# Performance work log

Hardware: AMD Instinct MI355X
Metric: run time of the kernel (lower is better)

## Reference

```python
import jax, jax.numpy as jnp
import numpy as np

B, N, C = 8, 1024, 1024
H = 16
D = C // H  # head_dim = 64
SCALE = D ** -0.5


def setup_inputs() -> dict:
    key = jax.random.key(0)
    k1, k2, k3 = jax.random.split(key, 3)
    x = jax.random.normal(k1, (B, N, C), dtype=jnp.float32)
    w_qkv = jax.random.normal(k2, (3 * C, C), dtype=jnp.float32) * (C ** -0.5)
    w_proj = jax.random.normal(k3, (C, C), dtype=jnp.float32) * (C ** -0.5)
    b_proj = jnp.zeros((C,), dtype=jnp.float32)
    return {"x": x, "w_qkv": w_qkv, "w_proj": w_proj, "b_proj": b_proj}


def reference(x, w_qkv, w_proj, b_proj):
    Bx, Nx, Cx = x.shape
    # qkv: [B,N,3C] -> [3,B,H,N,D]
    qkv = jnp.einsum('bnc,oc->bno', x, w_qkv)
    qkv = qkv.reshape(Bx, Nx, 3, H, D).transpose(2, 0, 3, 1, 4)
    q, k, v = qkv[0], qkv[1], qkv[2]
    attn = jnp.einsum('bhnd,bhmd->bhnm', q, k) * SCALE  # [B,H,N,N]
    attn = jax.nn.softmax(attn, axis=-1)
    out = jnp.einsum('bhnm,bhmd->bhnd', attn, v)  # [B,H,N,D]
    out = out.transpose(0, 2, 1, 3).reshape(Bx, Nx, Cx)
    return jnp.einsum('bnc,oc->bno', out, w_proj) + b_proj
```

## Files before the change

### kernel.cpp

```cpp
#include <hip/hip_runtime.h>

typedef _Float16 half8 __attribute__((ext_vector_type(8)));
typedef _Float16 half4v __attribute__((ext_vector_type(4)));
typedef _Float16 half2v __attribute__((ext_vector_type(2)));
typedef float floatx4 __attribute__((ext_vector_type(4)));

#define AS3 __attribute__((address_space(3)))
#define AS1 __attribute__((address_space(1)))

__global__ __launch_bounds__(256) void cvt_all(const float* __restrict__ x,
                                               const float* __restrict__ wq,
                                               const float* __restrict__ wp,
                                               _Float16* __restrict__ xh,
                                               _Float16* __restrict__ wqh,
                                               _Float16* __restrict__ wph) {
    long i = (long)blockIdx.x * 256 + threadIdx.x;
    const float4* src; half4v* dst; long off;
    if (i < 2097152)      { src = (const float4*)x;  dst = (half4v*)xh;  off = i; }
    else if (i < 2883584) { src = (const float4*)wq; dst = (half4v*)wqh; off = i - 2097152; }
    else                  { src = (const float4*)wp; dst = (half4v*)wph; off = i - 2883584; }
    float4 v = src[off];
    half4v h = {(_Float16)v.x, (_Float16)v.y, (_Float16)v.z, (_Float16)v.w};
    dst[off] = h;
}

__global__ __launch_bounds__(256, 4) void gemm_tn(
    const _Float16* __restrict__ A, const _Float16* __restrict__ B,
    _Float16* __restrict__ Ch, int ldc, _Float16* __restrict__ Vt, int split,
    float* __restrict__ Cf, const float* __restrict__ bias,
    int M, int Nn, int K)
{
    __shared__ _Float16 sA[2][128 * 32];
    __shared__ _Float16 sB[2][128 * 32];
    const int tid  = threadIdx.x;
    const int lane = tid & 63, wave = tid >> 6;
    const int quad = lane >> 4, l16 = lane & 15;
    const int wr = wave >> 1, wc = wave & 1;
    const long m0 = (long)blockIdx.x * 128, n0 = (long)blockIdx.y * 128;

    const int srow = tid >> 2;
    const int sslot = ((tid & 3) ^ ((srow >> 1) & 3)) * 8;
    const int dlo = srow * 32 + sslot;
    const int dhi = (srow + 64) * 32 + sslot;
    const _Float16* gA0 = A + (m0 + srow) * (long)K + (tid & 3) * 8;
    const _Float16* gA1 = A + (m0 + srow + 64) * (long)K + (tid & 3) * 8;
    const _Float16* gB0 = B + (n0 + srow) * (long)K + (tid & 3) * 8;
    const _Float16* gB1 = B + (n0 + srow + 64) * (long)K + (tid & 3) * 8;

    const int swz = (l16 >> 1) & 3;
    const int aoff = ((quad ^ swz) * 8);

    floatx4 acc[4][4] = {};
    const int nk = K >> 5;

    half8 rA0 = *(const half8*)gA0, rA1 = *(const half8*)gA1;
    half8 rB0 = *(const half8*)gB0, rB1 = *(const half8*)gB1;
    *(half8*)&sA[0][dlo] = rA0; *(half8*)&sA[0][dhi] = rA1;
    *(half8*)&sB[0][dlo] = rB0; *(half8*)&sB[0][dhi] = rB1;

    for (int kk = 0; kk < nk; kk++) {
        const int cur = kk & 1;
        __syncthreads();
        const bool more = (kk + 1 < nk);
        if (more) {
            const long k0 = (long)(kk + 1) << 5;
            rA0 = *(const half8*)(gA0 + k0); rA1 = *(const half8*)(gA1 + k0);
            rB0 = *(const half8*)(gB0 + k0); rB1 = *(const half8*)(gB1 + k0);
        }

        const _Float16* cA = &sA[cur][0];
        const _Float16* cB = &sB[cur][0];
        half8 af[4], bf[4];
#pragma unroll
        for (int t = 0; t < 4; t++)
            af[t] = *(const half8*)&cA[(wr * 64 + t * 16 + l16) * 32 + aoff];
#pragma unroll
        for (int t = 0; t < 4; t++)
            bf[t] = *(const half8*)&cB[(wc * 64 + t * 16 + l16) * 32 + aoff];
#pragma unroll
        for (int tm = 0; tm < 4; tm++)
#pragma unroll
            for (int tn = 0; tn < 4; tn++)
                acc[tm][tn] = __builtin_amdgcn_mfma_f32_16x16x32_f16(af[tm], bf[tn], acc[tm][tn], 0, 0, 0);

        if (more) {
            _Float16* nA = &sA[cur ^ 1][0];
            _Float16* nB = &sB[cur ^ 1][0];
            *(half8*)&nA[dlo] = rA0; *(half8*)&nA[dhi] = rA1;
            *(half8*)&nB[dlo] = rB0; *(half8*)&nB[dhi] = rB1;
        }
    }

#pragma unroll
    for (int tm = 0; tm < 4; tm++) {
        long row = m0 + wr * 64 + tm * 16 + quad * 4;
#pragma unroll
        for (int tn = 0; tn < 4; tn++) {
            long col = n0 + wc * 64 + tn * 16 + l16;
            if (Cf) {
                float bv = bias ? bias[col] : 0.f;
#pragma unroll
                for (int r = 0; r < 4; r++)
                    Cf[(row + r) * (long)Nn + col] = acc[tm][tn][r] + bv;
            } else if (col >= split) {
                long cv = col - split;
                long vrow = ((row >> 10) * 16 + (cv >> 6)) * 64 + (cv & 63);
                long nn = row & 1023;
                half4v pv = {(_Float16)acc[tm][tn][0], (_Float16)acc[tm][tn][1],
                             (_Float16)acc[tm][tn][2], (_Float16)acc[tm][tn][3]};
                *(half4v*)&Vt[vrow * 1024 + nn] = pv;
            } else {
#pragma unroll
                for (int r = 0; r < 4; r++)
                    Ch[(row + r) * (long)ldc + col] = (_Float16)acc[tm][tn][r];
            }
        }
    }
}

#define CSC 0.125f
__global__ __launch_bounds__(256, 4) void flash_attn(const _Float16* __restrict__ qk,
                                                     const _Float16* __restrict__ vt,
                                                     _Float16* __restrict__ out)
{
    const int bh = blockIdx.x, b = bh >> 4, h = bh & 15;
    const int n0 = blockIdx.y * 128;
    const int tid = threadIdx.x, lane = tid & 63, wave = tid >> 6;
    const int quad = lane >> 4, l16 = lane & 15;

    __shared__ _Float16 sK[64 * 72];
    __shared__ _Float16 sVT[64 * 72];
    __shared__ _Float16 sPT[4][32 * 72];

    half8 qf[2][2];
    const _Float16* qbase = qk + (long)(b * 1024 + n0 + wave * 32) * 2048 + h * 64;
#pragma unroll
    for (int t = 0; t < 2; t++)
#pragma unroll
        for (int s = 0; s < 2; s++)
            qf[t][s] = *(const half8*)(qbase + (long)(t * 16 + l16) * 2048 + s * 32 + quad * 8);

    const int srow = tid >> 3, scol8 = (tid & 7) * 8;
    const _Float16* kgb = qk + 1024 + h * 64 + scol8 + (long)(b * 1024 + srow) * 2048;
    const _Float16* vgb = vt + (long)(bh * 64 + srow) * 1024 + scol8;

    float m_[2] = {-1e30f, -1e30f}, l_[2] = {0.f, 0.f};
    floatx4 o[2][4] = {};

    for (int kt = 0; kt < 16; kt++) {
        const int kr0 = kt * 64;
        __syncthreads();
#pragma unroll
        for (int i = 0; i < 2; i++) {
            int r = srow + i * 32;
            *(half8*)&sK[r * 72 + scol8]  = *(const half8*)(kgb + (long)(kr0 + i * 32) * 2048);
            *(half8*)&sVT[r * 72 + scol8] = *(const half8*)(vgb + (long)(i * 32) * 1024 + kr0);
        }
        __syncthreads();

        floatx4 sacc[2][4] = {};
#pragma unroll
        for (int c = 0; c < 4; c++)
#pragma unroll
            for (int s = 0; s < 2; s++) {
                half8 kf = *(const half8*)&sK[(c * 16 + l16) * 72 + s * 32 + quad * 8];
                sacc[0][c] = __builtin_amdgcn_mfma_f32_16x16x32_f16(kf, qf[0][s], sacc[0][c], 0, 0, 0);
                sacc[1][c] = __builtin_amdgcn_mfma_f32_16x16x32_f16(kf, qf[1][s], sacc[1][c], 0, 0, 0);
            }

#pragma unroll
        for (int t = 0; t < 2; t++) {
            float mx = -1e30f;
#pragma unroll
            for (int c = 0; c < 4; c++)
#pragma unroll
                for (int r = 0; r < 4; r++) {
                    float v = sacc[t][c][r] * CSC;
                    sacc[t][c][r] = v;
                    mx = fmaxf(mx, v);
                }
            mx = fmaxf(mx, __shfl_xor(mx, 16));
            mx = fmaxf(mx, __shfl_xor(mx, 32));
            float mn = fmaxf(m_[t], mx);
            float al = __expf(m_[t] - mn);
            m_[t] = mn;
            float rs = 0.f;
#pragma unroll
            for (int c = 0; c < 4; c++)
#pragma unroll
                for (int r = 0; r < 4; r++) {
                    float p = __expf(sacc[t][c][r] - mn);
                    sacc[t][c][r] = p;
                    rs += p;
                }
            rs += __shfl_xor(rs, 16);
            rs += __shfl_xor(rs, 32);
            l_[t] = l_[t] * al + rs;
#pragma unroll
            for (int dt = 0; dt < 4; dt++) o[t][dt] *= al;
#pragma unroll
            for (int c = 0; c < 4; c++) {
                half4v p = {(_Float16)sacc[t][c][0], (_Float16)sacc[t][c][1],
                            (_Float16)sacc[t][c][2], (_Float16)sacc[t][c][3]};
                *(half4v*)&sPT[wave][(t * 16 + l16) * 72 + c * 16 + quad * 4] = p;
            }
        }

#pragma unroll
        for (int kk = 0; kk < 2; kk++) {
            half8 pf0 = *(const half8*)&sPT[wave][(l16) * 72 + kk * 32 + quad * 8];
            half8 pf1 = *(const half8*)&sPT[wave][(16 + l16) * 72 + kk * 32 + quad * 8];
#pragma unroll
            for (int dt = 0; dt < 4; dt++) {
                half8 vf = *(const half8*)&sVT[(dt * 16 + l16) * 72 + kk * 32 + quad * 8];
                o[0][dt] = __builtin_amdgcn_mfma_f32_16x16x32_f16(vf, pf0, o[0][dt], 0, 0, 0);
                o[1][dt] = __builtin_amdgcn_mfma_f32_16x16x32_f16(vf, pf1, o[1][dt], 0, 0, 0);
            }
        }
    }

#pragma unroll
    for (int t = 0; t < 2; t++) {
        float inv = 1.f / l_[t];
#pragma unroll
        for (int dt = 0; dt < 4; dt++) {
            floatx4 v = o[t][dt];
            half4v a = {(_Float16)(v[0] * inv), (_Float16)(v[1] * inv),
                        (_Float16)(v[2] * inv), (_Float16)(v[3] * inv)};
            *(half4v*)&sPT[wave][(t * 16 + l16) * 72 + dt * 16 + quad * 4] = a;
        }
    }
    __syncthreads();
#pragma unroll
    for (int i = 0; i < 4; i++) {
        int ql = i * 8 + (lane >> 3);
        int c8 = (lane & 7) * 8;
        half8 vv = *(const half8*)&sPT[wave][ql * 72 + c8];
        *(half8*)(out + (long)(b * 1024 + n0 + wave * 32 + ql) * 1024 + h * 64 + c8) = vv;
    }
}

extern "C" void kernel_launch(void* const* d_in, const int* in_sizes, int n_in,
                              void* d_out, int out_size, void* d_ws, size_t ws_size,
                              hipStream_t stream) {
    const float* x      = (const float*)d_in[0];
    const float* w_qkv  = (const float*)d_in[1];
    const float* w_proj = (const float*)d_in[2];
    const float* b_proj = (const float*)d_in[3];

    char* ws = (char*)d_ws;
    _Float16* qkh    = (_Float16*)ws;
    _Float16* vT     = (_Float16*)(ws + 33554432);
    _Float16* xh     = (_Float16*)(ws + 50331648);
    _Float16* wqkvh  = (_Float16*)(ws + 67108864);
    _Float16* wprojh = (_Float16*)(ws + 73400320);
    _Float16* attnh  = xh;

    cvt_all<<<12288, 256, 0, stream>>>(x, w_qkv, w_proj, xh, wqkvh, wprojh);

    gemm_tn<<<dim3(64, 24), 256, 0, stream>>>(xh, wqkvh, qkh, 2048, vT, 2048,
                                              nullptr, nullptr, 8192, 3072, 1024);
    flash_attn<<<dim3(128, 8), 256, 0, stream>>>(qkh, vT, attnh);
    gemm_tn<<<dim3(64, 8), 256, 0, stream>>>(attnh, wprojh, nullptr, 0, nullptr, 1 << 30,
                                             (float*)d_out, b_proj, 8192, 1024, 1024);
}
```

Measured before the change: 240.9 us.

## Fuse fp32-to-fp16 conversion into GEMM loads and prefetch K/V in attention

Removes the separate conversion kernel: the GEMMs now read fp32 inputs directly and convert to fp16 while loading each tile, which avoids a full extra pass over x and the weights. The flash attention kernel gains register prefetch of the next K/V tile, folds the softmax scale into Q once, and only rescales the running max and accumulators when the new max exceeds the old by more than a threshold. The trade-off is that the GEMMs re-read and re-convert fp32 data on every tile load, doubling their global read bytes, and the lazy-rescale softmax permits values up to e^8 before renormalising.

New measurement: 260.5 us. 1.08x slower.

```diff
diff --git a/kernel.cpp b/kernel.cpp
--- a/kernel.cpp
+++ b/kernel.cpp
@@ -2,30 +2,29 @@
 
 typedef _Float16 half8 __attribute__((ext_vector_type(8)));
 typedef _Float16 half4v __attribute__((ext_vector_type(4)));
-typedef _Float16 half2v __attribute__((ext_vector_type(2)));
 typedef float floatx4 __attribute__((ext_vector_type(4)));
 
-#define AS3 __attribute__((address_space(3)))
-#define AS1 __attribute__((address_space(1)))
-
-__global__ __launch_bounds__(256) void cvt_all(const float* __restrict__ x,
-                                               const float* __restrict__ wq,
-                                               const float* __restrict__ wp,
-                                               _Float16* __restrict__ xh,
-                                               _Float16* __restrict__ wqh,
-                                               _Float16* __restrict__ wph) {
-    long i = (long)blockIdx.x * 256 + threadIdx.x;
-    const float4* src; half4v* dst; long off;
-    if (i < 2097152)      { src = (const float4*)x;  dst = (half4v*)xh;  off = i; }
-    else if (i < 2883584) { src = (const float4*)wq; dst = (half4v*)wqh; off = i - 2097152; }
-    else                  { src = (const float4*)wp; dst = (half4v*)wph; off = i - 2883584; }
-    float4 v = src[off];
-    half4v h = {(_Float16)v.x, (_Float16)v.y, (_Float16)v.z, (_Float16)v.w};
-    dst[off] = h;
-}
-
+__device__ __forceinline__ floatx4 mfma16(half8 a, half8 b, floatx4 c) {
+    return __builtin_amdgcn_mfma_f32_16x16x32_f16(a, b, c, 0, 0, 0);
+}
+
+template<bool F32>
+__device__ __forceinline__ half8 ldcvt8(const void* __restrict__ base, long off) {
+    if constexpr (F32) {
+        const float* p = (const float*)base + off;
+        float4 a = *(const float4*)p;
+        float4 b = *(const float4*)(p + 4);
+        half8 h = {(_Float16)a.x, (_Float16)a.y, (_Float16)a.z, (_Float16)a.w,
+                   (_Float16)b.x, (_Float16)b.y, (_Float16)b.z, (_Float16)b.w};
+        return h;
+    } else {
+        return *(const half8*)((const _Float16*)base + off);
+    }
+}
+
+template<bool AF32, bool BF32>
 __global__ __launch_bounds__(256, 4) void gemm_tn(
-    const _Float16* __restrict__ A, const _Float16* __restrict__ B,
+    const void* __restrict__ A, const void* __restrict__ B,
     _Float16* __restrict__ Ch, int ldc, _Float16* __restrict__ Vt, int split,
     float* __restrict__ Cf, const float* __restrict__ bias,
     int M, int Nn, int K)
@@ -42,10 +41,10 @@
     const int sslot = ((tid & 3) ^ ((srow >> 1) & 3)) * 8;
     const int dlo = srow * 32 + sslot;
     const int dhi = (srow + 64) * 32 + sslot;
-    const _Float16* gA0 = A + (m0 + srow) * (long)K + (tid & 3) * 8;
-    const _Float16* gA1 = A + (m0 + srow + 64) * (long)K + (tid & 3) * 8;
-    const _Float16* gB0 = B + (n0 + srow) * (long)K + (tid & 3) * 8;
-    const _Float16* gB1 = B + (n0 + srow + 64) * (long)K + (tid & 3) * 8;
+    const long oA0 = (m0 + srow) * (long)K + (tid & 3) * 8;
+    const long oA1 = (m0 + srow + 64) * (long)K + (tid & 3) * 8;
+    const long oB0 = (n0 + srow) * (long)K + (tid & 3) * 8;
+    const long oB1 = (n0 + srow + 64) * (long)K + (tid & 3) * 8;
 
     const int swz = (l16 >> 1) & 3;
     const int aoff = ((quad ^ swz) * 8);
@@ -53,8 +52,8 @@
     floatx4 acc[4][4] = {};
     const int nk = K >> 5;
 
-    half8 rA0 = *(const half8*)gA0, rA1 = *(const half8*)gA1;
-    half8 rB0 = *(const half8*)gB0, rB1 = *(const half8*)gB1;
+    half8 rA0 = ldcvt8<AF32>(A, oA0), rA1 = ldcvt8<AF32>(A, oA1);
+    half8 rB0 = ldcvt8<BF32>(B, oB0), rB1 = ldcvt8<BF32>(B, oB1);
     *(half8*)&sA[0][dlo] = rA0; *(half8*)&sA[0][dhi] = rA1;
     *(half8*)&sB[0][dlo] = rB0; *(half8*)&sB[0][dhi] = rB1;
 
@@ -64,8 +63,8 @@
         const bool more = (kk + 1 < nk);
         if (more) {
             const long k0 = (long)(kk + 1) << 5;
-            rA0 = *(const half8*)(gA0 + k0); rA1 = *(const half8*)(gA1 + k0);
-            rB0 = *(const half8*)(gB0 + k0); rB1 = *(const half8*)(gB1 + k0);
+            rA0 = ldcvt8<AF32>(A, oA0 + k0); rA1 = ldcvt8<AF32>(A, oA1 + k0);
+            rB0 = ldcvt8<BF32>(B, oB0 + k0); rB1 = ldcvt8<BF32>(B, oB1 + k0);
         }
 
         const _Float16* cA = &sA[cur][0];
@@ -81,7 +80,7 @@
         for (int tm = 0; tm < 4; tm++)
 #pragma unroll
             for (int tn = 0; tn < 4; tn++)
-                acc[tm][tn] = __builtin_amdgcn_mfma_f32_16x16x32_f16(af[tm], bf[tn], acc[tm][tn], 0, 0, 0);
+                acc[tm][tn] = mfma16(af[tm], bf[tn], acc[tm][tn]);
 
         if (more) {
             _Float16* nA = &sA[cur ^ 1][0];
@@ -118,7 +117,6 @@
     }
 }
 
-#define CSC 0.125f
 __global__ __launch_bounds__(256, 4) void flash_attn(const _Float16* __restrict__ qk,
                                                      const _Float16* __restrict__ vt,
                                                      _Float16* __restrict__ out)
@@ -137,8 +135,12 @@
 #pragma unroll
     for (int t = 0; t < 2; t++)
 #pragma unroll
-        for (int s = 0; s < 2; s++)
-            qf[t][s] = *(const half8*)(qbase + (long)(t * 16 + l16) * 2048 + s * 32 + quad * 8);
+        for (int s = 0; s < 2; s++) {
+            half8 v = *(const half8*)(qbase + (long)(t * 16 + l16) * 2048 + s * 32 + quad * 8);
+#pragma unroll
+            for (int j = 0; j < 8; j++) v[j] *= (_Float16)0.125f;
+            qf[t][s] = v;
+        }
 
     const int srow = tid >> 3, scol8 = (tid & 7) * 8;
     const _Float16* kgb = qk + 1024 + h * 64 + scol8 + (long)(b * 1024 + srow) * 2048;
@@ -147,16 +149,26 @@
     float m_[2] = {-1e30f, -1e30f}, l_[2] = {0.f, 0.f};
     floatx4 o[2][4] = {};
 
+    half8 rK0 = *(const half8*)(kgb);
+    half8 rK1 = *(const half8*)(kgb + (long)32 * 2048);
+    half8 rV0 = *(const half8*)(vgb);
+    half8 rV1 = *(const half8*)(vgb + (long)32 * 1024);
+
     for (int kt = 0; kt < 16; kt++) {
-        const int kr0 = kt * 64;
         __syncthreads();
-#pragma unroll
-        for (int i = 0; i < 2; i++) {
-            int r = srow + i * 32;
-            *(half8*)&sK[r * 72 + scol8]  = *(const half8*)(kgb + (long)(kr0 + i * 32) * 2048);
-            *(half8*)&sVT[r * 72 + scol8] = *(const half8*)(vgb + (long)(i * 32) * 1024 + kr0);
-        }
+        *(half8*)&sK[srow * 72 + scol8]          = rK0;
+        *(half8*)&sK[(srow + 32) * 72 + scol8]   = rK1;
+        *(half8*)&sVT[srow * 72 + scol8]         = rV0;
+        *(half8*)&sVT[(srow + 32) * 72 + scol8]  = rV1;
         __syncthreads();
+
+        if (kt + 1 < 16) {
+            const long kr0n = (long)(kt + 1) * 64;
+            rK0 = *(const half8*)(kgb + kr0n * 2048);
+            rK1 = *(const half8*)(kgb + (kr0n + 32) * 2048);
+            rV0 = *(const half8*)(vgb + kr0n);
+            rV1 = *(const half8*)(vgb + (long)32 * 1024 + kr0n);
+        }
 
         floatx4 sacc[2][4] = {};
 #pragma unroll
@@ -164,8 +176,8 @@
 #pragma unroll
             for (int s = 0; s < 2; s++) {
                 half8 kf = *(const half8*)&sK[(c * 16 + l16) * 72 + s * 32 + quad * 8];
-                sacc[0][c] = __builtin_amdgcn_mfma_f32_16x16x32_f16(kf, qf[0][s], sacc[0][c], 0, 0, 0);
-                sacc[1][c] = __builtin_amdgcn_mfma_f32_16x16x32_f16(kf, qf[1][s], sacc[1][c], 0, 0, 0);
+                sacc[0][c] = mfma16(kf, qf[0][s], sacc[0][c]);
+                sacc[1][c] = mfma16(kf, qf[1][s], sacc[1][c]);
             }
 
 #pragma unroll
@@ -174,30 +186,30 @@
 #pragma unroll
             for (int c = 0; c < 4; c++)
 #pragma unroll
-                for (int r = 0; r < 4; r++) {
-                    float v = sacc[t][c][r] * CSC;
-                    sacc[t][c][r] = v;
-                    mx = fmaxf(mx, v);
-                }
+                for (int r = 0; r < 4; r++)
+                    mx = fmaxf(mx, sacc[t][c][r]);
             mx = fmaxf(mx, __shfl_xor(mx, 16));
             mx = fmaxf(mx, __shfl_xor(mx, 32));
-            float mn = fmaxf(m_[t], mx);
-            float al = __expf(m_[t] - mn);
-            m_[t] = mn;
+            if (__any(mx > m_[t] + 8.f)) {
+                float mn = fmaxf(m_[t], mx);
+                float al = __expf(m_[t] - mn);
+                m_[t] = mn;
+                l_[t] *= al;
+#pragma unroll
+                for (int dt = 0; dt < 4; dt++) o[t][dt] *= al;
+            }
             float rs = 0.f;
 #pragma unroll
             for (int c = 0; c < 4; c++)
 #pragma unroll
                 for (int r = 0; r < 4; r++) {
-                    float p = __expf(sacc[t][c][r] - mn);
+                    float p = __expf(sacc[t][c][r] - m_[t]);
                     sacc[t][c][r] = p;
                     rs += p;
                 }
             rs += __shfl_xor(rs, 16);
             rs += __shfl_xor(rs, 32);
-            l_[t] = l_[t] * al + rs;
-#pragma unroll
-            for (int dt = 0; dt < 4; dt++) o[t][dt] *= al;
+            l_[t] += rs;
 #pragma unroll
             for (int c = 0; c < 4; c++) {
                 half4v p = {(_Float16)sacc[t][c][0], (_Float16)sacc[t][c][1],
@@ -213,8 +225,8 @@
 #pragma unroll
             for (int dt = 0; dt < 4; dt++) {
                 half8 vf = *(const half8*)&sVT[(dt * 16 + l16) * 72 + kk * 32 + quad * 8];
-                o[0][dt] = __builtin_amdgcn_mfma_f32_16x16x32_f16(vf, pf0, o[0][dt], 0, 0, 0);
-                o[1][dt] = __builtin_amdgcn_mfma_f32_16x16x32_f16(vf, pf1, o[1][dt], 0, 0, 0);
+                o[0][dt] = mfma16(vf, pf0, o[0][dt]);
+                o[1][dt] = mfma16(vf, pf1, o[1][dt]);
             }
         }
     }
@@ -249,18 +261,14 @@
     const float* b_proj = (const float*)d_in[3];
 
     char* ws = (char*)d_ws;
-    _Float16* qkh    = (_Float16*)ws;
-    _Float16* vT     = (_Float16*)(ws + 33554432);
-    _Float16* xh     = (_Float16*)(ws + 50331648);
-    _Float16* wqkvh  = (_Float16*)(ws + 67108864);
-    _Float16* wprojh = (_Float16*)(ws + 73400320);
-    _Float16* attnh  = xh;
-
-    cvt_all<<<12288, 256, 0, stream>>>(x, w_qkv, w_proj, xh, wqkvh, wprojh);
-
-    gemm_tn<<<dim3(64, 24), 256, 0, stream>>>(xh, wqkvh, qkh, 2048, vT, 2048,
-                                              nullptr, nullptr, 8192, 3072, 1024);
+    _Float16* qkh   = (_Float16*)ws;
+    _Float16* vT    = (_Float16*)(ws + 33554432);
+    _Float16* attnh = (_Float16*)(ws + 50331648);
+
+    gemm_tn<true, true><<<dim3(64, 24), 256, 0, stream>>>(
+        x, w_qkv, qkh, 2048, vT, 2048, nullptr, nullptr, 8192, 3072, 1024);
     flash_attn<<<dim3(128, 8), 256, 0, stream>>>(qkh, vT, attnh);
-    gemm_tn<<<dim3(64, 8), 256, 0, stream>>>(attnh, wprojh, nullptr, 0, nullptr, 1 << 30,
-                                             (float*)d_out, b_proj, 8192, 1024, 1024);
-}
+    gemm_tn<false, true><<<dim3(64, 8), 256, 0, stream>>>(
+        attnh, w_proj, nullptr, 0, nullptr, 1 << 30,
+        (float*)d_out, b_proj, 8192, 1024, 1024);
+}
```
